# Kernel tuning notes

Hardware: AMD Instinct MI355X
Metric: run time of the kernel (lower is better)

The kernel has to match this reference:

```python
import jax, jax.numpy as jnp
import numpy as np

N_NODES = 49
FEAT_DIM = 1280            # efficientnet_v2_s feature dim
NODE_DIM = FEAT_DIM // N_NODES  # 26
GAT_HID = 256
HEADS = 4
NUM_CLASSES = 5
BATCH = 8192


def _grid_edges():
    # 7x7 grid, 8-neighborhood, as in _create_grid_edges, plus PyG default self loops
    edges = []
    for i in range(7):
        for j in range(7):
            node = i * 7 + j
            for di in (-1, 0, 1):
                for dj in (-1, 0, 1):
                    if di == 0 and dj == 0:
                        continue
                    ni, nj = i + di, j + dj
                    if 0 <= ni < 7 and 0 <= nj < 7:
                        edges.append((node, ni * 7 + nj))
    edges += [(n, n) for n in range(N_NODES)]  # add_self_loops=True (PyG default)
    return np.asarray(edges, dtype=np.int64).T  # [2, 361]


def setup_inputs() -> dict:
    key = jax.random.key(0)
    ks = jax.random.split(key, 16)
    s = 0.05
    inp = {
        "x": jax.random.normal(ks[0], (BATCH, FEAT_DIM), jnp.float32),
        "transform_w": jax.random.normal(ks[1], (FEAT_DIM, N_NODES * NODE_DIM), jnp.float32) * s,
        "transform_b": jnp.zeros((N_NODES * NODE_DIM,), jnp.float32),
        # GATv2 layer 1: 26 -> 64 per head, 4 heads, concat -> 256
        "g1_wl": jax.random.normal(ks[2], (NODE_DIM, GAT_HID), jnp.float32) * s,
        "g1_wr": jax.random.normal(ks[3], (NODE_DIM, GAT_HID), jnp.float32) * s,
        "g1_att": jax.random.normal(ks[4], (HEADS, GAT_HID // HEADS), jnp.float32) * s,
        "g1_b": jnp.zeros((GAT_HID,), jnp.float32),
        # GATv2 layer 2: 256 -> 256, 1 head, mean
        "g2_wl": jax.random.normal(ks[5], (GAT_HID, GAT_HID), jnp.float32) * s,
        "g2_wr": jax.random.normal(ks[6], (GAT_HID, GAT_HID), jnp.float32) * s,
        "g2_att": jax.random.normal(ks[7], (1, GAT_HID), jnp.float32) * s,
        "g2_b": jnp.zeros((GAT_HID,), jnp.float32),
        "fc_w": jax.random.normal(ks[8], (NODE_DIM + GAT_HID, NUM_CLASSES), jnp.float32) * s,
        "fc_b": jnp.zeros((NUM_CLASSES,), jnp.float32),
        "edge_index": jnp.asarray(_grid_edges()),
    }
    return inp


def _gatv2(x, src, dst, wl, wr, att, b, heads, out_ch, concat):
    # PyG GATv2Conv (share_weights=False, negative_slope=0.2, eval mode)
    n = x.shape[0]
    xl = (x @ wl).reshape(n, heads, out_ch)  # source messages
    xr = (x @ wr).reshape(n, heads, out_ch)  # target side of attention
    e = jax.nn.leaky_relu(xl[src] + xr[dst], 0.2)        # [E, H, C]
    score = jnp.einsum('ehc,hc->eh', e, att)             # [E, H]
    smax = jax.ops.segment_max(score, dst, num_segments=n)
    ex = jnp.exp(score - smax[dst])
    den = jax.ops.segment_sum(ex, dst, num_segments=n)
    alpha = ex / den[dst]                                # softmax over in-edges per node
    out = jax.ops.segment_sum(xl[src] * alpha[..., None], dst, num_segments=n)  # [N,H,C]
    out = out.reshape(n, heads * out_ch) if concat else out.mean(axis=1)
    return out + b


def reference(x, transform_w, transform_b, g1_wl, g1_wr, g1_att, g1_b,
              g2_wl, g2_wr, g2_att, g2_b, fc_w, fc_b, edge_index):
    src, dst = edge_index[0], edge_index[1]
    node = (x @ transform_w + transform_b).reshape(-1, N_NODES, NODE_DIM)  # [B,49,26]

    def graph(nf):
        h = _gatv2(nf, src, dst, g1_wl, g1_wr, g1_att, g1_b, HEADS, GAT_HID // HEADS, True)
        h = jax.nn.elu(h)  # dropout inactive in eval
        h = _gatv2(h, src, dst, g2_wl, g2_wr, g2_att, g2_b, 1, GAT_HID, False)
        return h  # [49, 256]

    g = jax.vmap(graph)(node)                              # [B,49,256]
    pooled = jnp.concatenate([node, g], axis=-1).mean(axis=1)  # [B, 282]
    return pooled @ fc_w + fc_b
```

## Files before the change

kernel.cpp:

```cpp
#include <hip/hip_runtime.h>
#include <hip/hip_bf16.h>

typedef __bf16 bf16;
typedef __attribute__((ext_vector_type(8))) __bf16 bf16x8;
typedef __attribute__((ext_vector_type(4))) float f32x4;

constexpr int BATCH = 8192, NN = 49, ND = 26, NOUT = 1274, FD = 1280;
constexpr int HID = 256, NE = 361, HEADS = 4;
constexpr int KT_X = 40;
constexpr int MT_X = 512;
constexpr int NB_W = 10;
constexpr int NTB  = 9;

constexpr size_t OFF_XPACK = 0;
constexpr size_t SZ_XPACK  = (size_t)MT_X * KT_X * 512 * 2;
constexpr size_t OFF_WPACK = OFF_XPACK + SZ_XPACK;
constexpr size_t SZ_WPACK  = (size_t)NB_W * NTB * KT_X * 512 * 2;
constexpr size_t OFF_B1    = OFF_WPACK + SZ_WPACK;
constexpr size_t SZ_B1     = (size_t)32 * 512 * 2;
constexpr size_t OFF_B2    = OFF_B1 + SZ_B1;
constexpr size_t SZ_B2     = (size_t)32 * 8 * 512 * 2;
constexpr size_t OFF_N32   = OFF_B2 + SZ_B2;
constexpr size_t SZ_N32    = (size_t)BATCH * NN * 32 * 2;
constexpr size_t OFF_PN    = OFF_N32 + SZ_N32;
constexpr size_t SZ_PN     = (size_t)BATCH * ND * 4;
constexpr size_t OFF_CSR   = OFF_PN + SZ_PN;
constexpr size_t SZ_CSR    = 8192;
constexpr size_t OFF_CHUNK = OFF_CSR + SZ_CSR;


__global__ __launch_bounds__(256) void k_pack_x(const float* __restrict__ x,
                                                bf16* __restrict__ xp) {
    int g = blockIdx.x * 256 + threadIdx.x;
    int lane = g & 63, frag = g >> 6;
    int mt = frag / KT_X, kt = frag - mt * KT_X;
    int row = mt * 16 + (lane & 15);
    int k0  = kt * 32 + (lane >> 4) * 8;
    const float* src = x + (size_t)row * FD + k0;
    bf16x8 v;
#pragma unroll
    for (int j = 0; j < 8; ++j) v[j] = (bf16)src[j];
    *(bf16x8*)(xp + ((size_t)frag * 64 + lane) * 8) = v;
}

__global__ __launch_bounds__(256) void k_pack_w(const float* __restrict__ w,
                                                bf16* __restrict__ wp) {
    int g = blockIdx.x * 256 + threadIdx.x;
    int lane = g & 63, frag = g >> 6;
    int kt = frag % KT_X, t2 = frag / KT_X;
    int nt = t2 % NTB, nb = t2 / NTB;
    int col = nb * 130 + nt * 16 + (lane & 15);
    int k0  = kt * 32 + (lane >> 4) * 8;
    bool ok = (col < NOUT) && (col < nb * 130 + 130);
    bf16x8 v;
#pragma unroll
    for (int j = 0; j < 8; ++j)
        v[j] = ok ? (bf16)w[(size_t)(k0 + j) * NOUT + col] : (bf16)0.f;
    *(bf16x8*)(wp + ((size_t)frag * 64 + lane) * 8) = v;
}

__global__ __launch_bounds__(256) void k_pack_g1(const float* __restrict__ wl,
                                                 const float* __restrict__ wr,
                                                 bf16* __restrict__ bp) {
    int g = blockIdx.x * 256 + threadIdx.x;
    int lane = g & 63, nt = g >> 6;
    int n  = nt * 16 + (lane & 15);
    int k0 = (lane >> 4) * 8;
    bf16x8 v;
#pragma unroll
    for (int j = 0; j < 8; ++j) {
        int k = k0 + j;
        float f = 0.f;
        if (k < ND) f = (n < HID) ? wl[k * HID + n] : wr[k * HID + (n - HID)];
        v[j] = (bf16)f;
    }
    *(bf16x8*)(bp + ((size_t)nt * 64 + lane) * 8) = v;
}

__global__ __launch_bounds__(256) void k_pack_g2(const float* __restrict__ wl,
                                                 const float* __restrict__ wr,
                                                 bf16* __restrict__ bp) {
    int g = blockIdx.x * 256 + threadIdx.x;
    int lane = g & 63, frag = g >> 6;
    int nt = frag >> 3, kt = frag & 7;
    int n  = nt * 16 + (lane & 15);
    int k0 = kt * 32 + (lane >> 4) * 8;
    bf16x8 v;
#pragma unroll
    for (int j = 0; j < 8; ++j) {
        int k = k0 + j;
        float f = (n < HID) ? wl[k * HID + n] : wr[k * HID + (n - HID)];
        v[j] = (bf16)f;
    }
    *(bf16x8*)(bp + ((size_t)frag * 64 + lane) * 8) = v;
}

__global__ __launch_bounds__(128) void k_csr_par(const int* __restrict__ ei,
                                                 int* __restrict__ csr) {
    __shared__ int es[NE], ed[NE], cnt[NN], ocnt[NN], off[NN + 1], ooff[NN + 1];
    int tid = threadIdx.x;
    if (tid < NN) { cnt[tid] = 0; ocnt[tid] = 0; }
    for (int e = tid; e < NE; e += 128) { es[e] = ei[e]; ed[e] = ei[NE + e]; }
    __syncthreads();
    for (int e = tid; e < NE; e += 128) {
        atomicAdd(&cnt[ed[e]], 1);
        atomicAdd(&ocnt[es[e]], 1);
    }
    __syncthreads();
    if (tid == 0) {
        off[0] = 0; ooff[0] = 0;
        for (int n = 0; n < NN; ++n) {
            off[n + 1] = off[n] + cnt[n];
            ooff[n + 1] = ooff[n] + ocnt[n];
        }
    }
    __syncthreads();
    if (tid < NN) {
        int p = off[tid];
        for (int e = 0; e < NE; ++e)
            if (ed[e] == tid) { csr[50 + p] = e; csr[411 + p] = es[e]; ++p; }
    } else if (tid >= 64 && tid < 64 + NN) {
        int n = tid - 64;
        int p = ooff[n];
        for (int e = 0; e < NE; ++e)
            if (es[e] == n) { csr[822 + p] = e; ++p; }
    }
    if (tid < 50) { csr[tid] = off[tid]; csr[772 + tid] = ooff[tid]; }
}

__global__ __launch_bounds__(256) void k_gemm_node(const bf16* __restrict__ xp,
                                                   const bf16* __restrict__ wp,
                                                   const float* __restrict__ tb,
                                                   bf16* __restrict__ node32) {
    __shared__ bf16 L[128][148];
    __shared__ float tbS[144];
    int tid = threadIdx.x, lane = tid & 63, w = tid >> 6;
    int nb = blockIdx.y, C0 = nb * 130;
    int mt0 = blockIdx.x * 8 + w * 2;
    if (tid < 144) { int col = C0 + tid; tbS[tid] = (col < NOUT) ? tb[col] : 0.f; }
    f32x4 acc[2][9] = {};
    const bf16* wpB = wp + (size_t)(nb * NTB) * KT_X * 512;
    for (int kt = 0; kt < KT_X; ++kt) {
        bf16x8 a[2];
#pragma unroll
        for (int i = 0; i < 2; ++i)
            a[i] = *(const bf16x8*)(xp + (((size_t)(mt0 + i) * KT_X + kt) * 64 + lane) * 8);
#pragma unroll
        for (int j = 0; j < NTB; ++j) {
            bf16x8 b = *(const bf16x8*)(wpB + ((size_t)(j * KT_X + kt) * 64 + lane) * 8);
            acc[0][j] = __builtin_amdgcn_mfma_f32_16x16x32_bf16(a[0], b, acc[0][j], 0, 0, 0);
            acc[1][j] = __builtin_amdgcn_mfma_f32_16x16x32_bf16(a[1], b, acc[1][j], 0, 0, 0);
        }
    }
    __syncthreads();
    int c0 = lane & 15, r0 = (lane >> 4) * 4;
#pragma unroll
    for (int i = 0; i < 2; ++i) {
        int rowb = (w * 2 + i) * 16 + r0;
#pragma unroll
        for (int j = 0; j < NTB; ++j) {
            int col = j * 16 + c0;
            float bias = tbS[col];
#pragma unroll
            for (int r = 0; r < 4; ++r)
                L[rowb + r][col] = (bf16)(acc[i][j][r] + bias);
        }
    }
    __syncthreads();
    int nodes = (nb == 9) ? 4 : 5;
    int total = 128 * nodes * 4;
    int B0 = blockIdx.x * 128;
    for (int t = tid; t < total; t += 256) {
        int q = t & 3, t2 = t >> 2;
        int n_l = t2 % nodes, brow = t2 / nodes;
        bf16x8 o;
#pragma unroll
        for (int jj = 0; jj < 8; ++jj) {
            int d = q * 8 + jj;
            o[jj] = (d < ND) ? L[brow][n_l * 26 + d] : (bf16)0.f;
        }
        *(bf16x8*)(node32 + (((size_t)(B0 + brow) * NN + nb * 5 + n_l) * 32 + q * 8)) = o;
    }
}

__global__ __launch_bounds__(256) void k_pool(const bf16* __restrict__ node32,
                                              float* __restrict__ pN) {
    int b = blockIdx.x * 8 + (threadIdx.x >> 5);
    int d = threadIdx.x & 31;
    if (d >= ND) return;
    const bf16* base = node32 + (size_t)b * NN * 32 + d;
    float s = 0.f;
    for (int n = 0; n < NN; ++n) s += (float)base[n * 32];
    pN[b * ND + d] = s;
}

__global__ __launch_bounds__(512, 4) void k_fuse1(const bf16* __restrict__ n32,
                                                  const bf16* __restrict__ B1p,
                                                  bf16* __restrict__ h1f,
                                                  const float* __restrict__ att1,
                                                  const float* __restrict__ g1b,
                                                  const int* __restrict__ ei,
                                                  const int* __restrict__ csr) {
    __shared__ __align__(16) char X[NN * 1024];
    __shared__ __align__(16) float attS[256];
    __shared__ float sc[NE * 4], srden[NN * 4], bS[256];
    __shared__ int ieOff[50], ieId[NE], ieSrc[NE], srcS[NE], dstS[NE];

    int tid = threadIdx.x, lane = tid & 63, w = tid >> 6, g = blockIdx.x;

    for (int i = tid; i < 256; i += 512) { attS[i] = att1[i]; bS[i] = g1b[i]; }
    for (int i = tid; i < NE; i += 512) {
        srcS[i] = ei[i]; dstS[i] = ei[NE + i];
        ieId[i] = csr[50 + i]; ieSrc[i] = csr[411 + i];
    }
    if (tid < 50) ieOff[tid] = csr[tid];

    {
        int mt = w & 3, ng = w >> 2;
        int arow = mt * 16 + (lane & 15);
        bf16x8 a = {};
        if (arow < NN)
            a = *(const bf16x8*)(n32 + ((size_t)(g * NN + arow) * 32 + (lane >> 4) * 8));
        f32x4 acc[16];
#pragma unroll
        for (int j = 0; j < 16; ++j) {
            f32x4 z = {0.f, 0.f, 0.f, 0.f};
            bf16x8 b = *(const bf16x8*)(B1p + ((size_t)(ng * 16 + j) * 64 + lane) * 8);
            acc[j] = __builtin_amdgcn_mfma_f32_16x16x32_bf16(a, b, z, 0, 0, 0);
        }
        int c0 = lane & 15, r0 = (lane >> 4) * 4;
#pragma unroll
        for (int j = 0; j < 16; ++j) {
            int col = (ng * 16 + j) * 16 + c0;
#pragma unroll
            for (int r = 0; r < 4; ++r) {
                int n = mt * 16 + r0 + r;
                if (n < NN)
                    *(bf16*)(X + n * 1024 + ((col * 2) ^ ((n & 7) << 4))) = (bf16)acc[j][r];
            }
        }
    }
    __syncthreads();

    int rot = tid & 7;
    for (int task = tid; task < NE * 4; task += 512) {
        int h = task / NE, e = task - h * NE;
        int s = srcS[e], d = dstS[e];
        int sws = (s & 7) << 4, swd = (d & 7) << 4;
        const char* ps = X + s * 1024;
        const char* pd = X + d * 1024;
        float p = 0.f;
#pragma unroll
        for (int i = 0; i < 8; ++i) {
            int cc = ((i + rot) & 7) * 8;
            bf16x8 xl = *(const bf16x8*)(ps + (((h * 64 + cc) * 2) ^ sws));
            bf16x8 xr = *(const bf16x8*)(pd + (((256 + h * 64 + cc) * 2) ^ swd));
            float4 a0 = *(const float4*)(attS + h * 64 + cc);
            float4 a1 = *(const float4*)(attS + h * 64 + cc + 4);
            const float aa[8] = {a0.x, a0.y, a0.z, a0.w, a1.x, a1.y, a1.z, a1.w};
#pragma unroll
            for (int q = 0; q < 8; ++q) {
                float v = (float)xl[q] + (float)xr[q];
                v = v > 0.f ? v : 0.2f * v;
                p = fmaf(aa[q], v, p);
            }
        }
        sc[e * 4 + h] = p;
    }
    __syncthreads();
    for (int t = tid; t < NN * 4; t += 512) {
        int n = t >> 2, h = t & 3;
        float m = -1e30f;
        for (int j = ieOff[n]; j < ieOff[n + 1]; ++j) m = fmaxf(m, sc[ieId[j] * 4 + h]);
        float den = 0.f;
        for (int j = ieOff[n]; j < ieOff[n + 1]; ++j) {
            int idx = ieId[j] * 4 + h;
            float ex = __expf(sc[idx] - m);
            sc[idx] = ex; den += ex;
        }
        srden[t] = 1.f / den;
    }
    __syncthreads();
    for (int task = tid; task < NN * 32; task += 512) {
        int n = task >> 5, cb = task & 31;
        int ch0 = cb * 8, hh = cb >> 3;
        float a8[8] = {};
        int j0 = ieOff[n], j1 = ieOff[n + 1];
        for (int j = j0; j < j1; ++j) {
            float al = sc[ieId[j] * 4 + hh];
            int s = ieSrc[j];
            bf16x8 xv = *(const bf16x8*)(X + s * 1024 + ((ch0 * 2) ^ ((s & 7) << 4)));
#pragma unroll
            for (int q = 0; q < 8; ++q) a8[q] = fmaf(al, (float)xv[q], a8[q]);
        }
        float rs = srden[n * 4 + hh];
        bf16x8 o;
#pragma unroll
        for (int q = 0; q < 8; ++q) {
            float v = fmaf(a8[q], rs, bS[ch0 + q]);
            v = v > 0.f ? v : (__expf(v) - 1.f);
            o[q] = (bf16)v;
        }
        int kt = cb >> 2, kg = cb & 3;
        size_t addr = (((size_t)g * 32 + (n >> 4) * 8 + kt) * 64 + (n & 15) + 16 * kg) * 8;
        *(bf16x8*)(h1f + addr) = o;
    }
}

static __device__ __forceinline__ float waveReduceSum(float v) {
#pragma unroll
    for (int m = 32; m > 0; m >>= 1) v += __shfl_xor(v, m, 64);
    return v;
}

__global__ __launch_bounds__(512, 4) void k_fuse2(const bf16* __restrict__ h1f,
                                                  const bf16* __restrict__ B2p,
                                                  const float* __restrict__ pooledN,
                                                  const float* __restrict__ att2,
                                                  const float* __restrict__ g2b,
                                                  const float* __restrict__ fcw,
                                                  const float* __restrict__ fcb,
                                                  const int* __restrict__ ei,
                                                  const int* __restrict__ csr,
                                                  int graph_base,
                                                  float* __restrict__ out) {
    __shared__ __align__(16) char X[NN * 1024];
    __shared__ __align__(16) float attS[256];
    __shared__ float sc2[NE * 2], scE[NE], srdenN[NN], smaxN[NN], wS[NN];
    __shared__ float b2S[256], pA[256], pB[256], pool[288], fcwS[282 * 5];
    __shared__ int srcS[NE], dstS[NE], ieOff[50], ieId[NE], oOff[50], oId[NE];

    int tid = threadIdx.x, lane = tid & 63, w = tid >> 6, g = blockIdx.x;

    for (int i = tid; i < 256; i += 512) { attS[i] = att2[i]; b2S[i] = g2b[i]; }
    for (int i = tid; i < NE; i += 512) {
        srcS[i] = ei[i]; dstS[i] = ei[NE + i];
        ieId[i] = csr[50 + i]; oId[i] = csr[822 + i];
    }
    if (tid < 50) { ieOff[tid] = csr[tid]; oOff[tid] = csr[772 + tid]; }
    for (int i = tid; i < 282 * 5; i += 512) fcwS[i] = fcw[i];

    {
        int mt = w & 3, ng = w >> 2;
        f32x4 acc[16] = {};
        for (int kt = 0; kt < 8; ++kt) {
            bf16x8 a = *(const bf16x8*)(h1f + (((size_t)g * 32 + mt * 8 + kt) * 64 + lane) * 8);
#pragma unroll
            for (int j = 0; j < 16; ++j) {
                bf16x8 b = *(const bf16x8*)(B2p + (((size_t)(ng * 16 + j) * 8 + kt) * 64 + lane) * 8);
                acc[j] = __builtin_amdgcn_mfma_f32_16x16x32_bf16(a, b, acc[j], 0, 0, 0);
            }
        }
        int c0 = lane & 15, r0 = (lane >> 4) * 4;
#pragma unroll
        for (int j = 0; j < 16; ++j) {
            int col = (ng * 16 + j) * 16 + c0;
#pragma unroll
            for (int r = 0; r < 4; ++r) {
                int n = mt * 16 + r0 + r;
                if (n < NN)
                    *(bf16*)(X + n * 1024 + ((col * 2) ^ ((n & 7) << 4))) = (bf16)acc[j][r];
            }
        }
    }
    __syncthreads();

    int rot = tid & 7;
    for (int task = tid; task < NE * 2; task += 512) {
        int e = task >> 1, half = task & 1;
        int s = srcS[e], d = dstS[e];
        int sws = (s & 7) << 4, swd = (d & 7) << 4;
        const char* ps = X + s * 1024;
        const char* pd = X + d * 1024;
        float p = 0.f;
#pragma unroll
        for (int i = 0; i < 16; ++i) {
            int cc = half * 128 + (((i + rot) & 15)) * 8;
            bf16x8 xl = *(const bf16x8*)(ps + ((cc * 2) ^ sws));
            bf16x8 xr = *(const bf16x8*)(pd + (((256 + cc) * 2) ^ swd));
            float4 a0 = *(const float4*)(attS + cc);
            float4 a1 = *(const float4*)(attS + cc + 4);
            const float aa[8] = {a0.x, a0.y, a0.z, a0.w, a1.x, a1.y, a1.z, a1.w};
#pragma unroll
            for (int q = 0; q < 8; ++q) {
                float v = (float)xl[q] + (float)xr[q];
                v = v > 0.f ? v : 0.2f * v;
                p = fmaf(aa[q], v, p);
            }
        }
        sc2[task] = p;
    }
    __syncthreads();
    for (int e = tid; e < NE; e += 512) scE[e] = sc2[2 * e] + sc2[2 * e + 1];
    __syncthreads();
    for (int n = tid; n < NN; n += 512) {
        float m = -1e30f;
        for (int j = ieOff[n]; j < ieOff[n + 1]; ++j) m = fmaxf(m, scE[ieId[j]]);
        float den = 0.f;
        for (int j = ieOff[n]; j < ieOff[n + 1]; ++j) den += __expf(scE[ieId[j]] - m);
        smaxN[n] = m; srdenN[n] = 1.f / den;
    }
    __syncthreads();
    for (int n = tid; n < NN; n += 512) {
        float wacc = 0.f;
        for (int j = oOff[n]; j < oOff[n + 1]; ++j) {
            int e = oId[j], d = dstS[e];
            wacc += __expf(scE[e] - smaxN[d]) * srdenN[d];
        }
        wS[n] = wacc;
    }
    __syncthreads();
    {
        int ch = tid & 255, half = tid >> 8;
        int n0 = half ? 25 : 0, n1 = half ? NN : 25;
        float acc = 0.f;
        for (int n = n0; n < n1; ++n) {
            float v = (float)*(const bf16*)(X + n * 1024 + ((ch * 2) ^ ((n & 7) << 4)));
            acc = fmaf(wS[n], v, acc);
        }
        (half ? pB : pA)[ch] = acc;
    }
    __syncthreads();
    if (tid < ND) pool[tid] = pooledN[(size_t)(graph_base + g) * ND + tid] * (1.f / NN);
    else if (tid >= 32 && tid < 32 + HID) {
        int ch = tid - 32;
        pool[ND + ch] = (pA[ch] + pB[ch]) * (1.f / NN) + b2S[ch];
    }
    __syncthreads();
    int w5 = tid >> 6;
    if (w5 < 5) {
        float a = 0.f;
        for (int d = lane; d < ND + HID; d += 64) a = fmaf(pool[d], fcwS[d * 5 + w5], a);
        a = waveReduceSum(a);
        if (lane == 0) out[(size_t)(graph_base + g) * 5 + w5] = a + fcb[w5];
    }
}

extern "C" void kernel_launch(void* const* d_in, const int* in_sizes, int n_in,
                              void* d_out, int out_size, void* d_ws, size_t ws_size,
                              hipStream_t stream) {
    const float* x   = (const float*)d_in[0];
    const float* tw  = (const float*)d_in[1];
    const float* tb  = (const float*)d_in[2];
    const float* wl1 = (const float*)d_in[3];
    const float* wr1 = (const float*)d_in[4];
    const float* at1 = (const float*)d_in[5];
    const float* b1  = (const float*)d_in[6];
    const float* wl2 = (const float*)d_in[7];
    const float* wr2 = (const float*)d_in[8];
    const float* at2 = (const float*)d_in[9];
    const float* b2  = (const float*)d_in[10];
    const float* fcw = (const float*)d_in[11];
    const float* fcb = (const float*)d_in[12];
    const int*   ei  = (const int*)d_in[13];
    float* out = (float*)d_out;

    char* ws = (char*)d_ws;
    bf16*  xp   = (bf16*)(ws + OFF_XPACK);
    bf16*  wp   = (bf16*)(ws + OFF_WPACK);
    bf16*  b1p  = (bf16*)(ws + OFF_B1);
    bf16*  b2p  = (bf16*)(ws + OFF_B2);
    bf16*  n32  = (bf16*)(ws + OFF_N32);
    float* pN   = (float*)(ws + OFF_PN);
    int*   csr  = (int*)(ws + OFF_CSR);

    int C = 512;
    for (int cand : {2048, 1024, 512}) {
        if (OFF_CHUNK + (size_t)cand * 32768 <= ws_size) { C = cand; break; }
    }
    bf16* h1f = (bf16*)(ws + OFF_CHUNK);
    int nchunks = BATCH / C;

    k_pack_x<<<dim3(MT_X * KT_X * 64 / 256), dim3(256), 0, stream>>>(x, xp);
    k_pack_w<<<dim3(NB_W * NTB * KT_X * 64 / 256), dim3(256), 0, stream>>>(tw, wp);
    k_pack_g1<<<dim3(8), dim3(256), 0, stream>>>(wl1, wr1, b1p);
    k_pack_g2<<<dim3(64), dim3(256), 0, stream>>>(wl2, wr2, b2p);
    k_csr_par<<<dim3(1), dim3(128), 0, stream>>>(ei, csr);
    k_gemm_node<<<dim3(64, NB_W), dim3(256), 0, stream>>>(xp, wp, tb, n32);
    k_pool<<<dim3(BATCH / 8), dim3(256), 0, stream>>>(n32, pN);

    for (int c = 0; c < nchunks; ++c) {
        const bf16* n32c = n32 + (size_t)c * C * NN * 32;
        k_fuse1<<<dim3(C), dim3(512), 0, stream>>>(n32c, b1p, h1f, at1, b1, ei, csr);
        k_fuse2<<<dim3(C), dim3(512), 0, stream>>>(h1f, b2p, pN, at2, b2, fcw, fcb,
                                                   ei, csr, c * C, out);
    }
}
```

Measured before the change: 988.2 us.

## Split layer-2 GEMM into batched tiled kernel and enlarge node GEMM tiles

```diff
diff --git a/kernel.cpp b/kernel.cpp
--- a/kernel.cpp
+++ b/kernel.cpp
@@ -128,58 +128,63 @@
     if (tid < 50) { csr[tid] = off[tid]; csr[772 + tid] = ooff[tid]; }
 }
 
-__global__ __launch_bounds__(256) void k_gemm_node(const bf16* __restrict__ xp,
-                                                   const bf16* __restrict__ wp,
-                                                   const float* __restrict__ tb,
-                                                   bf16* __restrict__ node32) {
+__global__ __launch_bounds__(256, 2) void k_gemm_node(const bf16* __restrict__ xp,
+                                                      const bf16* __restrict__ wp,
+                                                      const float* __restrict__ tb,
+                                                      bf16* __restrict__ node32) {
     __shared__ bf16 L[128][148];
     __shared__ float tbS[144];
     int tid = threadIdx.x, lane = tid & 63, w = tid >> 6;
     int nb = blockIdx.y, C0 = nb * 130;
-    int mt0 = blockIdx.x * 8 + w * 2;
+    int mt0 = blockIdx.x * 16 + w * 4;
     if (tid < 144) { int col = C0 + tid; tbS[tid] = (col < NOUT) ? tb[col] : 0.f; }
-    f32x4 acc[2][9] = {};
+    f32x4 acc[4][9] = {};
     const bf16* wpB = wp + (size_t)(nb * NTB) * KT_X * 512;
     for (int kt = 0; kt < KT_X; ++kt) {
-        bf16x8 a[2];
-#pragma unroll
-        for (int i = 0; i < 2; ++i)
+        bf16x8 a[4];
+#pragma unroll
+        for (int i = 0; i < 4; ++i)
             a[i] = *(const bf16x8*)(xp + (((size_t)(mt0 + i) * KT_X + kt) * 64 + lane) * 8);
 #pragma unroll
         for (int j = 0; j < NTB; ++j) {
             bf16x8 b = *(const bf16x8*)(wpB + ((size_t)(j * KT_X + kt) * 64 + lane) * 8);
-            acc[0][j] = __builtin_amdgcn_mfma_f32_16x16x32_bf16(a[0], b, acc[0][j], 0, 0, 0);
-            acc[1][j] = __builtin_amdgcn_mfma_f32_16x16x32_bf16(a[1], b, acc[1][j], 0, 0, 0);
-        }
-    }
-    __syncthreads();
+#pragma unroll
+            for (int i = 0; i < 4; ++i)
+                acc[i][j] = __builtin_amdgcn_mfma_f32_16x16x32_bf16(a[i], b, acc[i][j], 0, 0, 0);
+        }
+    }
     int c0 = lane & 15, r0 = (lane >> 4) * 4;
-#pragma unroll
-    for (int i = 0; i < 2; ++i) {
-        int rowb = (w * 2 + i) * 16 + r0;
-#pragma unroll
-        for (int j = 0; j < NTB; ++j) {
-            int col = j * 16 + c0;
-            float bias = tbS[col];
-#pragma unroll
-            for (int r = 0; r < 4; ++r)
-                L[rowb + r][col] = (bf16)(acc[i][j][r] + bias);
-        }
-    }
-    __syncthreads();
     int nodes = (nb == 9) ? 4 : 5;
     int total = 128 * nodes * 4;
-    int B0 = blockIdx.x * 128;
-    for (int t = tid; t < total; t += 256) {
-        int q = t & 3, t2 = t >> 2;
-        int n_l = t2 % nodes, brow = t2 / nodes;
-        bf16x8 o;
-#pragma unroll
-        for (int jj = 0; jj < 8; ++jj) {
-            int d = q * 8 + jj;
-            o[jj] = (d < ND) ? L[brow][n_l * 26 + d] : (bf16)0.f;
-        }
-        *(bf16x8*)(node32 + (((size_t)(B0 + brow) * NN + nb * 5 + n_l) * 32 + q * 8)) = o;
+    for (int half = 0; half < 2; ++half) {
+        __syncthreads();
+        if ((w >> 1) == half) {
+            int lrbase = (w & 1) * 64;
+#pragma unroll
+            for (int i = 0; i < 4; ++i) {
+#pragma unroll
+                for (int j = 0; j < NTB; ++j) {
+                    int col = j * 16 + c0;
+                    float bias = tbS[col];
+#pragma unroll
+                    for (int r = 0; r < 4; ++r)
+                        L[lrbase + i * 16 + r0 + r][col] = (bf16)(acc[i][j][r] + bias);
+                }
+            }
+        }
+        __syncthreads();
+        int B0 = blockIdx.x * 256 + half * 128;
+        for (int t = tid; t < total; t += 256) {
+            int q = t & 3, t2 = t >> 2;
+            int n_l = t2 % nodes, brow = t2 / nodes;
+            bf16x8 o;
+#pragma unroll
+            for (int jj = 0; jj < 8; ++jj) {
+                int d = q * 8 + jj;
+                o[jj] = (d < ND) ? L[brow][n_l * 26 + d] : (bf16)0.f;
+            }
+            *(bf16x8*)(node32 + (((size_t)(B0 + brow) * NN + nb * 5 + n_l) * 32 + q * 8)) = o;
+        }
     }
 }
 
@@ -194,7 +199,7 @@
     pN[b * ND + d] = s;
 }
 
-__global__ __launch_bounds__(512, 4) void k_fuse1(const bf16* __restrict__ n32,
+__global__ __launch_bounds__(512, 2) void k_fuse1(const bf16* __restrict__ n32,
                                                   const bf16* __restrict__ B1p,
                                                   bf16* __restrict__ h1f,
                                                   const float* __restrict__ att1,
@@ -249,7 +254,7 @@
         int sws = (s & 7) << 4, swd = (d & 7) << 4;
         const char* ps = X + s * 1024;
         const char* pd = X + d * 1024;
-        float p = 0.f;
+        float pa[4] = {0.f, 0.f, 0.f, 0.f};
 #pragma unroll
         for (int i = 0; i < 8; ++i) {
             int cc = ((i + rot) & 7) * 8;
@@ -262,10 +267,10 @@
             for (int q = 0; q < 8; ++q) {
                 float v = (float)xl[q] + (float)xr[q];
                 v = v > 0.f ? v : 0.2f * v;
-                p = fmaf(aa[q], v, p);
+                pa[q & 3] = fmaf(aa[q], v, pa[q & 3]);
             }
         }
-        sc[e * 4 + h] = p;
+        sc[e * 4 + h] = (pa[0] + pa[1]) + (pa[2] + pa[3]);
     }
     __syncthreads();
     for (int t = tid; t < NN * 4; t += 512) {
@@ -301,9 +306,52 @@
             v = v > 0.f ? v : (__expf(v) - 1.f);
             o[q] = (bf16)v;
         }
-        int kt = cb >> 2, kg = cb & 3;
-        size_t addr = (((size_t)g * 32 + (n >> 4) * 8 + kt) * 64 + (n & 15) + 16 * kg) * 8;
+        int Rl = g * NN + n;
+        int kt = ch0 >> 5, kg = (ch0 >> 3) & 3;
+        size_t addr = (((size_t)(Rl >> 4) * 8 + kt) * 64 + (Rl & 15) + 16 * kg) * 8;
         *(bf16x8*)(h1f + addr) = o;
+    }
+}
+
+__global__ __launch_bounds__(256) void k_gemm_l2(const bf16* __restrict__ Af,
+                                                 const bf16* __restrict__ Bf,
+                                                 bf16* __restrict__ xlr) {
+    __shared__ bf16 LT[128][136];
+    int tid = threadIdx.x, lane = tid & 63, w = tid >> 6;
+    int mtb = blockIdx.x * 8 + (w >> 1) * 4;
+    int ntb = blockIdx.y * 8 + (w & 1) * 4;
+    f32x4 acc[4][4] = {};
+    for (int kt = 0; kt < 8; ++kt) {
+        bf16x8 a[4], b[4];
+#pragma unroll
+        for (int i = 0; i < 4; ++i)
+            a[i] = *(const bf16x8*)(Af + (((size_t)(mtb + i) * 8 + kt) * 64 + lane) * 8);
+#pragma unroll
+        for (int j = 0; j < 4; ++j)
+            b[j] = *(const bf16x8*)(Bf + (((size_t)(ntb + j) * 8 + kt) * 64 + lane) * 8);
+#pragma unroll
+        for (int i = 0; i < 4; ++i)
+#pragma unroll
+            for (int j = 0; j < 4; ++j)
+                acc[i][j] = __builtin_amdgcn_mfma_f32_16x16x32_bf16(a[i], b[j], acc[i][j], 0, 0, 0);
+    }
+    int c0 = lane & 15, r0 = (lane >> 4) * 4;
+    int lr0 = (w >> 1) * 64, lc0 = (w & 1) * 64;
+#pragma unroll
+    for (int i = 0; i < 4; ++i)
+#pragma unroll
+        for (int j = 0; j < 4; ++j)
+#pragma unroll
+            for (int r = 0; r < 4; ++r)
+                LT[lr0 + i * 16 + r0 + r][lc0 + j * 16 + c0] = (bf16)acc[i][j][r];
+    __syncthreads();
+    size_t R0 = (size_t)blockIdx.x * 128, C0 = (size_t)blockIdx.y * 128;
+#pragma unroll
+    for (int it = 0; it < 8; ++it) {
+        int idx = (it * 256 + tid) * 8;
+        int r = idx >> 7, c = idx & 127;
+        bf16x8 v = *(const bf16x8*)&LT[r][c];
+        *(bf16x8*)(xlr + (R0 + r) * 512 + C0 + c) = v;
     }
 }
 
@@ -313,8 +361,7 @@
     return v;
 }
 
-__global__ __launch_bounds__(512, 4) void k_fuse2(const bf16* __restrict__ h1f,
-                                                  const bf16* __restrict__ B2p,
+__global__ __launch_bounds__(512, 2) void k_edge2(const bf16* __restrict__ xlrG,
                                                   const float* __restrict__ pooledN,
                                                   const float* __restrict__ att2,
                                                   const float* __restrict__ g2b,
@@ -330,8 +377,12 @@
     __shared__ float b2S[256], pA[256], pB[256], pool[288], fcwS[282 * 5];
     __shared__ int srcS[NE], dstS[NE], ieOff[50], ieId[NE], oOff[50], oId[NE];
 
-    int tid = threadIdx.x, lane = tid & 63, w = tid >> 6, g = blockIdx.x;
-
+    int tid = threadIdx.x, g = blockIdx.x;
+    const char* srcp = (const char*)(xlrG + (size_t)g * NN * 512);
+    for (int off = tid * 16; off < NN * 1024; off += 512 * 16) {
+        int row = off >> 10;
+        *(uint4*)(X + (off ^ ((row & 7) << 4))) = *(const uint4*)(srcp + off);
+    }
     for (int i = tid; i < 256; i += 512) { attS[i] = att2[i]; b2S[i] = g2b[i]; }
     for (int i = tid; i < NE; i += 512) {
         srcS[i] = ei[i]; dstS[i] = ei[NE + i];
@@ -339,30 +390,6 @@
     }
     if (tid < 50) { ieOff[tid] = csr[tid]; oOff[tid] = csr[772 + tid]; }
     for (int i = tid; i < 282 * 5; i += 512) fcwS[i] = fcw[i];
-
-    {
-        int mt = w & 3, ng = w >> 2;
-        f32x4 acc[16] = {};
-        for (int kt = 0; kt < 8; ++kt) {
-            bf16x8 a = *(const bf16x8*)(h1f + (((size_t)g * 32 + mt * 8 + kt) * 64 + lane) * 8);
-#pragma unroll
-            for (int j = 0; j < 16; ++j) {
-                bf16x8 b = *(const bf16x8*)(B2p + (((size_t)(ng * 16 + j) * 8 + kt) * 64 + lane) * 8);
-                acc[j] = __builtin_amdgcn_mfma_f32_16x16x32_bf16(a, b, acc[j], 0, 0, 0);
-            }
-        }
-        int c0 = lane & 15, r0 = (lane >> 4) * 4;
-#pragma unroll
-        for (int j = 0; j < 16; ++j) {
-            int col = (ng * 16 + j) * 16 + c0;
-#pragma unroll
-            for (int r = 0; r < 4; ++r) {
-                int n = mt * 16 + r0 + r;
-                if (n < NN)
-                    *(bf16*)(X + n * 1024 + ((col * 2) ^ ((n & 7) << 4))) = (bf16)acc[j][r];
-            }
-        }
-    }
     __syncthreads();
 
     int rot = tid & 7;
@@ -372,7 +399,7 @@
         int sws = (s & 7) << 4, swd = (d & 7) << 4;
         const char* ps = X + s * 1024;
         const char* pd = X + d * 1024;
-        float p = 0.f;
+        float pa[4] = {0.f, 0.f, 0.f, 0.f};
 #pragma unroll
         for (int i = 0; i < 16; ++i) {
             int cc = half * 128 + (((i + rot) & 15)) * 8;
@@ -385,10 +412,10 @@
             for (int q = 0; q < 8; ++q) {
                 float v = (float)xl[q] + (float)xr[q];
                 v = v > 0.f ? v : 0.2f * v;
-                p = fmaf(aa[q], v, p);
+                pa[q & 3] = fmaf(aa[q], v, pa[q & 3]);
             }
         }
-        sc2[task] = p;
+        sc2[task] = (pa[0] + pa[1]) + (pa[2] + pa[3]);
     }
     __syncthreads();
     for (int e = tid; e < NE; e += 512) scE[e] = sc2[2 * e] + sc2[2 * e + 1];
@@ -427,7 +454,7 @@
         pool[ND + ch] = (pA[ch] + pB[ch]) * (1.f / NN) + b2S[ch];
     }
     __syncthreads();
-    int w5 = tid >> 6;
+    int w5 = tid >> 6, lane = tid & 63;
     if (w5 < 5) {
         float a = 0.f;
         for (int d = lane; d < ND + HID; d += 64) a = fmaf(pool[d], fcwS[d * 5 + w5], a);
@@ -466,23 +493,26 @@
 
     int C = 512;
     for (int cand : {2048, 1024, 512}) {
-        if (OFF_CHUNK + (size_t)cand * 32768 <= ws_size) { C = cand; break; }
-    }
-    bf16* h1f = (bf16*)(ws + OFF_CHUNK);
+        if (OFF_CHUNK + (size_t)cand * (50176 + 12544) <= ws_size) { C = cand; break; }
+    }
+    bf16* xlr = (bf16*)(ws + OFF_CHUNK);
+    bf16* h1f = (bf16*)(ws + OFF_CHUNK + (size_t)C * 50176);
     int nchunks = BATCH / C;
+    int MtC = C * NN / 16;
 
     k_pack_x<<<dim3(MT_X * KT_X * 64 / 256), dim3(256), 0, stream>>>(x, xp);
     k_pack_w<<<dim3(NB_W * NTB * KT_X * 64 / 256), dim3(256), 0, stream>>>(tw, wp);
     k_pack_g1<<<dim3(8), dim3(256), 0, stream>>>(wl1, wr1, b1p);
     k_pack_g2<<<dim3(64), dim3(256), 0, stream>>>(wl2, wr2, b2p);
     k_csr_par<<<dim3(1), dim3(128), 0, stream>>>(ei, csr);
-    k_gemm_node<<<dim3(64, NB_W), dim3(256), 0, stream>>>(xp, wp, tb, n32);
+    k_gemm_node<<<dim3(32, NB_W), dim3(256), 0, stream>>>(xp, wp, tb, n32);
     k_pool<<<dim3(BATCH / 8), dim3(256), 0, stream>>>(n32, pN);
 
     for (int c = 0; c < nchunks; ++c) {
         const bf16* n32c = n32 + (size_t)c * C * NN * 32;
         k_fuse1<<<dim3(C), dim3(512), 0, stream>>>(n32c, b1p, h1f, at1, b1, ei, csr);
-        k_fuse2<<<dim3(C), dim3(512), 0, stream>>>(h1f, b2p, pN, at2, b2, fcw, fcb,
+        k_gemm_l2<<<dim3(MtC / 8, 4), dim3(256), 0, stream>>>(h1f, b2p, xlr);
+        k_edge2<<<dim3(C), dim3(512), 0, stream>>>(xlr, pN, at2, b2, fcw, fcb,
                                                    ei, csr, c * C, out);
     }
 }
```

New measurement: 1.068 ms. 1.08x slower.
